# Optimization experiments

Hardware: AMD Instinct MI355X
Metric: run time of the kernel (lower is better)

## Reference

```python
import jax, jax.numpy as jnp
import numpy as np

SIGMA = 1.0
TOP_K = 4

def setup_inputs() -> dict:
    key = jax.random.key(0)
    k1, k2, k3, k4 = jax.random.split(key, 4)
    B, N, IN_DIM, OUT_DIM, P = 2, 4096, 128, 128, 3
    x = jax.random.normal(k1, (B, N, IN_DIM), dtype=jnp.float32)
    pos = jax.random.normal(k2, (B, N, P), dtype=jnp.float32)
    # Linear(in_dim, out_dim): W [in_dim, out_dim], b [out_dim]
    lim = 1.0 / np.sqrt(IN_DIM)
    W = jax.random.uniform(k3, (IN_DIM, OUT_DIM), minval=-lim, maxval=lim, dtype=jnp.float32)
    b = jax.random.uniform(k4, (OUT_DIM,), minval=-lim, maxval=lim, dtype=jnp.float32)
    return {"x": x, "pos": pos, "W": W, "b": b}

def reference(x, pos, W, b):
    B, N, _ = x.shape
    # pairwise distances [B, N, N]
    pos_diff = pos[:, :, None, :] - pos[:, None, :, :]
    dist = jnp.sqrt(jnp.sum(pos_diff ** 2, axis=-1) + 1e-8)
    adj = jnp.exp(-dist ** 2 / (2.0 * SIGMA ** 2))
    # top-k mask along last dim
    _, indices = jax.lax.top_k(adj, TOP_K)  # [B, N, k]
    b_idx = jnp.arange(B)[:, None, None]
    n_idx = jnp.arange(N)[None, :, None]
    mask = jnp.zeros_like(adj).at[b_idx, n_idx, indices].set(1.0)
    adj = adj * mask
    adj = adj / (jnp.sum(adj, axis=-1, keepdims=True) + 1e-8)
    # weighted aggregation + linear
    out = jnp.einsum('bnm,bmd->bnd', adj, x)
    return out @ W + b
```

## Files before the change

### kernel.cpp

```cpp
#include <hip/hip_runtime.h>
#include <hip/hip_bf16.h>

#define NPTS 4096
#define NROWS 8192
#define DIM 128
#define TILE 2048
#define GEMM_BLOCKS 1024

typedef __attribute__((ext_vector_type(8))) short bf16x8;
typedef __attribute__((ext_vector_type(4))) float f32x4;

__global__ __launch_bounds__(256) void xw_mfma(const float* __restrict__ x,
                                               const float* __restrict__ W,
                                               __hip_bfloat16* __restrict__ xWb) {
    int wave = threadIdx.x >> 6;
    int lane = threadIdx.x & 63;
    int tile = blockIdx.x * 4 + wave;
    int m0 = (tile >> 3) << 4;
    int n0 = (tile & 7) << 4;
    int r = lane & 15;
    int kg = lane >> 4;
    const float* xr = x + (size_t)(m0 + r) * DIM + kg * 8;
    const float* wc = W + (size_t)(kg * 8) * DIM + (n0 + r);
    f32x4 acc = {0.f, 0.f, 0.f, 0.f};
    union { __hip_bfloat16 h; short s; } u;
#pragma unroll
    for (int kb = 0; kb < 4; ++kb) {
        float4 a0 = *(const float4*)(xr + kb * 32);
        float4 a1 = *(const float4*)(xr + kb * 32 + 4);
        bf16x8 af, bf;
        u.h = __float2bfloat16(a0.x); af[0] = u.s;
        u.h = __float2bfloat16(a0.y); af[1] = u.s;
        u.h = __float2bfloat16(a0.z); af[2] = u.s;
        u.h = __float2bfloat16(a0.w); af[3] = u.s;
        u.h = __float2bfloat16(a1.x); af[4] = u.s;
        u.h = __float2bfloat16(a1.y); af[5] = u.s;
        u.h = __float2bfloat16(a1.z); af[6] = u.s;
        u.h = __float2bfloat16(a1.w); af[7] = u.s;
#pragma unroll
        for (int i = 0; i < 8; ++i) {
            u.h = __float2bfloat16(wc[(size_t)(kb * 32 + i) * DIM]);
            bf[i] = u.s;
        }
        acc = __builtin_amdgcn_mfma_f32_16x16x32_bf16(af, bf, acc, 0, 0, 0);
    }
    int col = n0 + r;
    int rbase = m0 + (kg << 2);
#pragma unroll
    for (int reg = 0; reg < 4; ++reg)
        xWb[(size_t)(rbase + reg) * DIM + col] = __float2bfloat16(acc[reg]);
}

__device__ __forceinline__ double mkkey(float d2, int j) {
    return __longlong_as_double(__double_as_longlong((double)d2) |
                                (unsigned long long)(unsigned)j);
}

__device__ __forceinline__ void kins(double& k0, double& k1, double& k2,
                                     double& k3, double s) {
    double c = fmax(k0, s); k0 = fmin(k0, s);
    double t = fmax(k1, c); k1 = fmin(k1, c); c = t;
    t = fmax(k2, c);        k2 = fmin(k2, c); c = t;
    k3 = fmin(k3, c);
}

__device__ __forceinline__ void kmerge(double& a0, double& a1, double& a2,
                                       double& a3, double b0, double b1,
                                       double b2, double b3) {
    double m0 = fmin(a0, b3), m1 = fmin(a1, b2);
    double m2 = fmin(a2, b1), m3 = fmin(a3, b0);
    double t0 = fmin(m0, m2), t2 = fmax(m0, m2);
    double t1 = fmin(m1, m3), t3 = fmax(m1, m3);
    a0 = fmin(t0, t1); a1 = fmax(t0, t1);
    a2 = fmin(t2, t3); a3 = fmax(t2, t3);
}

__global__ __launch_bounds__(256) void topk_agg(const float* __restrict__ pos,
                                                const __hip_bfloat16* __restrict__ xWb,
                                                const float* __restrict__ bias,
                                                float* __restrict__ out) {
    __shared__ float sp[TILE * 3];
    int lane = threadIdx.x & 63;
    int wave = threadIdx.x >> 6;
    int rowbase = blockIdx.x * 8;
    int batch = rowbase >> 12;
    int ibase = rowbase & (NPTS - 1);
    const float* pb = pos + (size_t)batch * NPTS * 3;

    int r0 = ibase + wave * 2;
    float q0x = pb[3 * r0 + 0], q0y = pb[3 * r0 + 1], q0z = pb[3 * r0 + 2];
    float q1x = pb[3 * r0 + 3], q1y = pb[3 * r0 + 4], q1z = pb[3 * r0 + 5];

    const double INF = __builtin_inf();
    double a0 = INF, a1 = INF, a2 = INF, a3 = INF;
    double b0 = INF, b1 = INF, b2 = INF, b3 = INF;

    for (int tile = 0; tile < 2; ++tile) {
        const float4* src = (const float4*)(pb + (size_t)tile * TILE * 3);
        float4* dst = (float4*)sp;
#pragma unroll
        for (int i = 0; i < 6; ++i)
            dst[threadIdx.x * 6 + i] = src[threadIdx.x * 6 + i];
        __syncthreads();

        int jb = tile * TILE + lane;
#pragma unroll 4
        for (int it = 0; it < TILE / 64; ++it) {
            int jj = it * 64 + lane;
            float px = sp[3 * jj + 0];
            float py = sp[3 * jj + 1];
            float pz = sp[3 * jj + 2];
            int j = jb + it * 64;
            float dx = q0x - px, dy = q0y - py, dz = q0z - pz;
            float d2 = fmaf(dx, dx, fmaf(dy, dy, dz * dz));
            kins(a0, a1, a2, a3, mkkey(d2, j));
            dx = q1x - px; dy = q1y - py; dz = q1z - pz;
            d2 = fmaf(dx, dx, fmaf(dy, dy, dz * dz));
            kins(b0, b1, b2, b3, mkkey(d2, j));
        }
        __syncthreads();
    }

#pragma unroll
    for (int off = 1; off < 64; off <<= 1) {
        double p0 = __shfl_xor(a0, off), p1 = __shfl_xor(a1, off);
        double p2 = __shfl_xor(a2, off), p3 = __shfl_xor(a3, off);
        kmerge(a0, a1, a2, a3, p0, p1, p2, p3);
        p0 = __shfl_xor(b0, off); p1 = __shfl_xor(b1, off);
        p2 = __shfl_xor(b2, off); p3 = __shfl_xor(b3, off);
        kmerge(b0, b1, b2, b3, p0, p1, p2, p3);
    }

    int c = lane << 1;
    float2 bb = *(const float2*)(bias + c);
    const unsigned short* xu = (const unsigned short*)xWb;
    size_t bbase = ((size_t)batch * NPTS) << 7;
#pragma unroll
    for (int k = 0; k < 2; ++k) {
        double k0 = k ? b0 : a0, k1 = k ? b1 : a1;
        double k2 = k ? b2 : a2, k3 = k ? b3 : a3;
        unsigned i0 = (unsigned)__double_as_longlong(k0) & 0xFFFu;
        unsigned i1 = (unsigned)__double_as_longlong(k1) & 0xFFFu;
        unsigned i2 = (unsigned)__double_as_longlong(k2) & 0xFFFu;
        unsigned i3 = (unsigned)__double_as_longlong(k3) & 0xFFFu;
        float d0 = (float)k0, d1 = (float)k1, d2 = (float)k2, d3 = (float)k3;
        float w0 = __expf(-(d0 + 1e-8f) * 0.5f);
        float w1 = __expf(-(d1 + 1e-8f) * 0.5f);
        float w2 = __expf(-(d2 + 1e-8f) * 0.5f);
        float w3 = __expf(-(d3 + 1e-8f) * 0.5f);
        float inv = 1.0f / (w0 + w1 + w2 + w3 + 1e-8f);
        w0 *= inv; w1 *= inv; w2 *= inv; w3 *= inv;
        ushort2 g0 = *(const ushort2*)(xu + bbase + ((size_t)i0 << 7) + c);
        ushort2 g1 = *(const ushort2*)(xu + bbase + ((size_t)i1 << 7) + c);
        ushort2 g2 = *(const ushort2*)(xu + bbase + ((size_t)i2 << 7) + c);
        ushort2 g3 = *(const ushort2*)(xu + bbase + ((size_t)i3 << 7) + c);
        float ox = bb.x + w0 * __uint_as_float((unsigned)g0.x << 16)
                        + w1 * __uint_as_float((unsigned)g1.x << 16)
                        + w2 * __uint_as_float((unsigned)g2.x << 16)
                        + w3 * __uint_as_float((unsigned)g3.x << 16);
        float oy = bb.y + w0 * __uint_as_float((unsigned)g0.y << 16)
                        + w1 * __uint_as_float((unsigned)g1.y << 16)
                        + w2 * __uint_as_float((unsigned)g2.y << 16)
                        + w3 * __uint_as_float((unsigned)g3.y << 16);
        *(float2*)(out + (((size_t)(rowbase + wave * 2 + k)) << 7) + c) =
            make_float2(ox, oy);
    }
}

extern "C" void kernel_launch(void* const* d_in, const int* in_sizes, int n_in,
                              void* d_out, int out_size, void* d_ws, size_t ws_size,
                              hipStream_t stream) {
    const float* x    = (const float*)d_in[0];
    const float* pos  = (const float*)d_in[1];
    const float* W    = (const float*)d_in[2];
    const float* bias = (const float*)d_in[3];
    float* out = (float*)d_out;

    __hip_bfloat16* xWb = (__hip_bfloat16*)d_ws;

    xw_mfma<<<GEMM_BLOCKS, 256, 0, stream>>>(x, W, xWb);
    topk_agg<<<NROWS / 8, 256, 0, stream>>>(pos, xWb, bias, out);
}
```

Before: 88.04 us.

## Fuse xW GEMM into top-k aggregation kernel, aggregate raw x then project

```diff
diff --git a/kernel.cpp b/kernel.cpp
--- a/kernel.cpp
+++ b/kernel.cpp
@@ -4,52 +4,10 @@
 #define NPTS 4096
 #define NROWS 8192
 #define DIM 128
-#define TILE 2048
-#define GEMM_BLOCKS 1024
+#define LSTRIDE 264
 
 typedef __attribute__((ext_vector_type(8))) short bf16x8;
 typedef __attribute__((ext_vector_type(4))) float f32x4;
-
-__global__ __launch_bounds__(256) void xw_mfma(const float* __restrict__ x,
-                                               const float* __restrict__ W,
-                                               __hip_bfloat16* __restrict__ xWb) {
-    int wave = threadIdx.x >> 6;
-    int lane = threadIdx.x & 63;
-    int tile = blockIdx.x * 4 + wave;
-    int m0 = (tile >> 3) << 4;
-    int n0 = (tile & 7) << 4;
-    int r = lane & 15;
-    int kg = lane >> 4;
-    const float* xr = x + (size_t)(m0 + r) * DIM + kg * 8;
-    const float* wc = W + (size_t)(kg * 8) * DIM + (n0 + r);
-    f32x4 acc = {0.f, 0.f, 0.f, 0.f};
-    union { __hip_bfloat16 h; short s; } u;
-#pragma unroll
-    for (int kb = 0; kb < 4; ++kb) {
-        float4 a0 = *(const float4*)(xr + kb * 32);
-        float4 a1 = *(const float4*)(xr + kb * 32 + 4);
-        bf16x8 af, bf;
-        u.h = __float2bfloat16(a0.x); af[0] = u.s;
-        u.h = __float2bfloat16(a0.y); af[1] = u.s;
-        u.h = __float2bfloat16(a0.z); af[2] = u.s;
-        u.h = __float2bfloat16(a0.w); af[3] = u.s;
-        u.h = __float2bfloat16(a1.x); af[4] = u.s;
-        u.h = __float2bfloat16(a1.y); af[5] = u.s;
-        u.h = __float2bfloat16(a1.z); af[6] = u.s;
-        u.h = __float2bfloat16(a1.w); af[7] = u.s;
-#pragma unroll
-        for (int i = 0; i < 8; ++i) {
-            u.h = __float2bfloat16(wc[(size_t)(kb * 32 + i) * DIM]);
-            bf[i] = u.s;
-        }
-        acc = __builtin_amdgcn_mfma_f32_16x16x32_bf16(af, bf, acc, 0, 0, 0);
-    }
-    int col = n0 + r;
-    int rbase = m0 + (kg << 2);
-#pragma unroll
-    for (int reg = 0; reg < 4; ++reg)
-        xWb[(size_t)(rbase + reg) * DIM + col] = __float2bfloat16(acc[reg]);
-}
 
 __device__ __forceinline__ double mkkey(float d2, int j) {
     return __longlong_as_double(__double_as_longlong((double)d2) |
@@ -75,17 +33,33 @@
     a2 = fmin(t2, t3); a3 = fmax(t2, t3);
 }
 
-__global__ __launch_bounds__(256) void topk_agg(const float* __restrict__ pos,
-                                                const __hip_bfloat16* __restrict__ xWb,
-                                                const float* __restrict__ bias,
-                                                float* __restrict__ out) {
-    __shared__ float sp[TILE * 3];
+__device__ __forceinline__ float bf2f(unsigned short u) {
+    return __uint_as_float((unsigned)u << 16);
+}
+
+__global__ __launch_bounds__(256) void gnn_fused(const float* __restrict__ x,
+                                                 const float* __restrict__ pos,
+                                                 const float* __restrict__ W,
+                                                 const float* __restrict__ bias,
+                                                 float* __restrict__ out) {
+    __shared__ unsigned short sW[64 * LSTRIDE];
+    __shared__ float sxa[4][2][DIM];
+
     int lane = threadIdx.x & 63;
     int wave = threadIdx.x >> 6;
     int rowbase = blockIdx.x * 8;
     int batch = rowbase >> 12;
     int ibase = rowbase & (NPTS - 1);
     const float* pb = pos + (size_t)batch * NPTS * 3;
+    const float* xb = x + (((size_t)batch * NPTS) << 7);
+
+    union { __hip_bfloat16 h; unsigned short u; } cv;
+    for (int e = threadIdx.x; e < DIM * DIM; e += 256) {
+        int k = e >> 7, c = e & 127;
+        cv.h = __float2bfloat16(W[e]);
+        sW[(c >> 1) * LSTRIDE + (c & 1) * DIM + k] = cv.u;
+    }
+    __syncthreads();
 
     int r0 = ibase + wave * 2;
     float q0x = pb[3 * r0 + 0], q0y = pb[3 * r0 + 1], q0z = pb[3 * r0 + 2];
@@ -95,32 +69,19 @@
     double a0 = INF, a1 = INF, a2 = INF, a3 = INF;
     double b0 = INF, b1 = INF, b2 = INF, b3 = INF;
 
-    for (int tile = 0; tile < 2; ++tile) {
-        const float4* src = (const float4*)(pb + (size_t)tile * TILE * 3);
-        float4* dst = (float4*)sp;
-#pragma unroll
-        for (int i = 0; i < 6; ++i)
-            dst[threadIdx.x * 6 + i] = src[threadIdx.x * 6 + i];
-        __syncthreads();
-
-        int jb = tile * TILE + lane;
-#pragma unroll 4
-        for (int it = 0; it < TILE / 64; ++it) {
-            int jj = it * 64 + lane;
-            float px = sp[3 * jj + 0];
-            float py = sp[3 * jj + 1];
-            float pz = sp[3 * jj + 2];
-            int j = jb + it * 64;
-            float dx = q0x - px, dy = q0y - py, dz = q0z - pz;
-            float d2 = fmaf(dx, dx, fmaf(dy, dy, dz * dz));
-            kins(a0, a1, a2, a3, mkkey(d2, j));
-            dx = q1x - px; dy = q1y - py; dz = q1z - pz;
-            d2 = fmaf(dx, dx, fmaf(dy, dy, dz * dz));
-            kins(b0, b1, b2, b3, mkkey(d2, j));
-        }
-        __syncthreads();
+#pragma unroll 8
+    for (int it = 0; it < NPTS / 64; ++it) {
+        int j = it * 64 + lane;
+        float px = pb[3 * j + 0];
+        float py = pb[3 * j + 1];
+        float pz = pb[3 * j + 2];
+        float dx = q0x - px, dy = q0y - py, dz = q0z - pz;
+        float d2 = fmaf(dx, dx, fmaf(dy, dy, dz * dz));
+        kins(a0, a1, a2, a3, mkkey(d2, j));
+        dx = q1x - px; dy = q1y - py; dz = q1z - pz;
+        d2 = fmaf(dx, dx, fmaf(dy, dy, dz * dz));
+        kins(b0, b1, b2, b3, mkkey(d2, j));
     }
-
 #pragma unroll
     for (int off = 1; off < 64; off <<= 1) {
         double p0 = __shfl_xor(a0, off), p1 = __shfl_xor(a1, off);
@@ -132,9 +93,6 @@
     }
 
     int c = lane << 1;
-    float2 bb = *(const float2*)(bias + c);
-    const unsigned short* xu = (const unsigned short*)xWb;
-    size_t bbase = ((size_t)batch * NPTS) << 7;
 #pragma unroll
     for (int k = 0; k < 2; ++k) {
         double k0 = k ? b0 : a0, k1 = k ? b1 : a1;
@@ -150,21 +108,43 @@
         float w3 = __expf(-(d3 + 1e-8f) * 0.5f);
         float inv = 1.0f / (w0 + w1 + w2 + w3 + 1e-8f);
         w0 *= inv; w1 *= inv; w2 *= inv; w3 *= inv;
-        ushort2 g0 = *(const ushort2*)(xu + bbase + ((size_t)i0 << 7) + c);
-        ushort2 g1 = *(const ushort2*)(xu + bbase + ((size_t)i1 << 7) + c);
-        ushort2 g2 = *(const ushort2*)(xu + bbase + ((size_t)i2 << 7) + c);
-        ushort2 g3 = *(const ushort2*)(xu + bbase + ((size_t)i3 << 7) + c);
-        float ox = bb.x + w0 * __uint_as_float((unsigned)g0.x << 16)
-                        + w1 * __uint_as_float((unsigned)g1.x << 16)
-                        + w2 * __uint_as_float((unsigned)g2.x << 16)
-                        + w3 * __uint_as_float((unsigned)g3.x << 16);
-        float oy = bb.y + w0 * __uint_as_float((unsigned)g0.y << 16)
-                        + w1 * __uint_as_float((unsigned)g1.y << 16)
-                        + w2 * __uint_as_float((unsigned)g2.y << 16)
-                        + w3 * __uint_as_float((unsigned)g3.y << 16);
-        *(float2*)(out + (((size_t)(rowbase + wave * 2 + k)) << 7) + c) =
-            make_float2(ox, oy);
+        float2 g0 = *(const float2*)(xb + ((size_t)i0 << 7) + c);
+        float2 g1 = *(const float2*)(xb + ((size_t)i1 << 7) + c);
+        float2 g2 = *(const float2*)(xb + ((size_t)i2 << 7) + c);
+        float2 g3 = *(const float2*)(xb + ((size_t)i3 << 7) + c);
+        float ax = w0 * g0.x + w1 * g1.x + w2 * g2.x + w3 * g3.x;
+        float ay = w0 * g0.y + w1 * g1.y + w2 * g2.y + w3 * g3.y;
+        sxa[wave][k][c] = ax;
+        sxa[wave][k][c + 1] = ay;
     }
+
+    const unsigned short* wl = sW + (size_t)lane * LSTRIDE;
+    float o0x = 0.f, o0y = 0.f, o1x = 0.f, o1y = 0.f;
+#pragma unroll 4
+    for (int kb = 0; kb < DIM / 8; ++kb) {
+        bf16x8 wc0 = *(const bf16x8*)(wl + kb * 8);
+        bf16x8 wc1 = *(const bf16x8*)(wl + DIM + kb * 8);
+        f32x4 xr0a = *(const f32x4*)(&sxa[wave][0][kb * 8]);
+        f32x4 xr0b = *(const f32x4*)(&sxa[wave][0][kb * 8 + 4]);
+        f32x4 xr1a = *(const f32x4*)(&sxa[wave][1][kb * 8]);
+        f32x4 xr1b = *(const f32x4*)(&sxa[wave][1][kb * 8 + 4]);
+#pragma unroll
+        for (int i = 0; i < 4; ++i) {
+            float wa = bf2f((unsigned short)wc0[i]);
+            float wb = bf2f((unsigned short)wc0[i + 4]);
+            float va = bf2f((unsigned short)wc1[i]);
+            float vb = bf2f((unsigned short)wc1[i + 4]);
+            o0x = fmaf(xr0a[i], wa, o0x); o0x = fmaf(xr0b[i], wb, o0x);
+            o0y = fmaf(xr0a[i], va, o0y); o0y = fmaf(xr0b[i], vb, o0y);
+            o1x = fmaf(xr1a[i], wa, o1x); o1x = fmaf(xr1b[i], wb, o1x);
+            o1y = fmaf(xr1a[i], va, o1y); o1y = fmaf(xr1b[i], vb, o1y);
+        }
+    }
+    float2 bb = *(const float2*)(bias + c);
+    *(float2*)(out + (((size_t)(rowbase + wave * 2 + 0)) << 7) + c) =
+        make_float2(o0x + bb.x, o0y + bb.y);
+    *(float2*)(out + (((size_t)(rowbase + wave * 2 + 1)) << 7) + c) =
+        make_float2(o1x + bb.x, o1y + bb.y);
 }
 
 extern "C" void kernel_launch(void* const* d_in, const int* in_sizes, int n_in,
@@ -176,8 +156,5 @@
     const float* bias = (const float*)d_in[3];
     float* out = (float*)d_out;
 
-    __hip_bfloat16* xWb = (__hip_bfloat16*)d_ws;
-
-    xw_mfma<<<GEMM_BLOCKS, 256, 0, stream>>>(x, W, xWb);
-    topk_agg<<<NROWS / 8, 256, 0, stream>>>(pos, xWb, bias, out);
+    gnn_fused<<<NROWS / 8, 256, 0, stream>>>(x, pos, W, bias, out);
 }
```

Measured after the change: 88.77 us. No clear change (+0.8%).
